# Kernel tuning notes

Measured on AMD Instinct MI355X. Metric: run time of the kernel, lower is better.

The kernel has to match this reference:

```python
import jax, jax.numpy as jnp
import numpy as np

H = 256      # HIDDEN_DIM
F_IN = 16    # input_dim
B = 512
S = 168      # encoder sequence length
T = 24       # PRED_LEN


def _lstm_cell(x, h, c, w_ih, w_hh, b):
    # torch gate order: i, f, g, o
    g = x @ w_ih.T + h @ w_hh.T + b
    i, f, gg, o = jnp.split(g, 4, axis=-1)
    c_new = jax.nn.sigmoid(f) * c + jax.nn.sigmoid(i) * jnp.tanh(gg)
    h_new = jax.nn.sigmoid(o) * jnp.tanh(c_new)
    return h_new, c_new


def _lstm_layer(x, w_ih, w_hh, b):
    # x: [S, B, in] -> outputs [S, B, H], final (h, c)
    Bv, Hv = x.shape[1], w_hh.shape[1]
    init = (jnp.zeros((Bv, Hv), x.dtype), jnp.zeros((Bv, Hv), x.dtype))
    def step(carry, xt):
        h, c = _lstm_cell(xt, carry[0], carry[1], w_ih, w_hh, b)
        return (h, c), h
    (h, c), ys = jax.lax.scan(step, init, x)
    return ys, h, c


def setup_inputs() -> dict:
    key = jax.random.key(0)
    ks = jax.random.split(key, 24)
    s = 1.0 / np.sqrt(H)
    u = lambda k, shape: jax.random.uniform(k, shape, jnp.float32, -s, s)
    inp = {}
    inp['src'] = jax.random.normal(ks[0], (B, S, F_IN), jnp.float32)
    # encoder LSTM (2 layers); biases b_ih + b_hh fused into one vector
    inp['enc_w_ih0'] = u(ks[1], (4 * H, F_IN))
    inp['enc_w_hh0'] = u(ks[2], (4 * H, H))
    inp['enc_b0'] = u(ks[3], (4 * H,))
    inp['enc_w_ih1'] = u(ks[4], (4 * H, H))
    inp['enc_w_hh1'] = u(ks[5], (4 * H, H))
    inp['enc_b1'] = u(ks[6], (4 * H,))
    # decoder LSTM (2 layers), input_size = 1 + H
    inp['dec_w_ih0'] = u(ks[7], (4 * H, 1 + H))
    inp['dec_w_hh0'] = u(ks[8], (4 * H, H))
    inp['dec_b0'] = u(ks[9], (4 * H,))
    inp['dec_w_ih1'] = u(ks[10], (4 * H, H))
    inp['dec_w_hh1'] = u(ks[11], (4 * H, H))
    inp['dec_b1'] = u(ks[12], (4 * H,))
    # attention: Linear(2H -> H), v: Linear(H -> 1, no bias), position bias
    inp['attn_w'] = u(ks[13], (H, 2 * H))
    inp['attn_b'] = u(ks[14], (H,))
    inp['attn_v'] = u(ks[15], (H,))
    inp['pos_bias'] = jax.random.normal(ks[16], (H,), jnp.float32)
    # fc_out: Linear(H -> 1)
    inp['fc_w'] = u(ks[17], (1, H))
    inp['fc_b'] = u(ks[18], (1,))
    return inp


def reference(src, enc_w_ih0, enc_w_hh0, enc_b0, enc_w_ih1, enc_w_hh1, enc_b1,
              dec_w_ih0, dec_w_hh0, dec_b0, dec_w_ih1, dec_w_hh1, dec_b1,
              attn_w, attn_b, attn_v, pos_bias, fc_w, fc_b):
    x = jnp.transpose(src, (1, 0, 2))  # [S, B, F]
    y0, _, _ = _lstm_layer(x, enc_w_ih0, enc_w_hh0, enc_b0)
    enc_out_t, h1e, c1e = _lstm_layer(y0, enc_w_ih1, enc_w_hh1, enc_b1)
    # also need final state of layer 0 for decoder init
    h0e, c0e = y0[-1], None
    # recompute layer-0 final cell state: rerun scan carry output
    # (cheap alternative: _lstm_layer returns (ys, h, c); reuse it)
    _, h0e, c0e = _lstm_layer(x, enc_w_ih0, enc_w_hh0, enc_b0)
    enc_out = jnp.transpose(enc_out_t, (1, 0, 2))  # [B, S, H]

    We, Wd = attn_w[:, :H], attn_w[:, H:]
    enc_proj = jnp.einsum('bsh,gh->bsg', enc_out, We)  # precomputed encoder projection
    dec_in0 = src[:, -1, -1:]  # [B, 1]

    def dec_step(carry, t):
        h0, c0, h1, c1, dec_in = carry
        # additive attention using top-layer decoder hidden
        e = jnp.tanh(enc_proj + (h1 @ Wd.T + attn_b)[:, None, :])
        e = e + pos_bias[None, None, :] * (t / 24.0)
        w = jax.nn.softmax(e @ attn_v, axis=1)              # [B, S]
        ctx = jnp.einsum('bs,bsh->bh', w, enc_out)          # [B, H]
        x0 = jnp.concatenate([dec_in, ctx], axis=1)          # [B, 1+H]
        h0n, c0n = _lstm_cell(x0, h0, c0, dec_w_ih0, dec_w_hh0, dec_b0)
        h1n, c1n = _lstm_cell(h0n, h1, c1, dec_w_ih1, dec_w_hh1, dec_b1)
        pred = h1n @ fc_w.T + fc_b                           # [B, 1]
        # NOTE: the gated blend of decoder_output in the source is dead code
        # (the blended tensor is never used), so it is omitted here.
        return (h0n, c0n, h1n, c1n, pred), pred

    ts = jnp.arange(T, dtype=src.dtype)
    _, preds = jax.lax.scan(dec_step, (h0e, c0e, h1e, c1e, dec_in0), ts)
    return jnp.transpose(preds, (1, 0, 2))  # [B, T, 1]
```

## Files before the change

kernel.cpp:

```cpp
#include <hip/hip_runtime.h>
#include <hip/hip_fp16.h>
#include <math.h>

#define BB 512
#define HH 256
#define SS 168
#define TT 24
#define NBLK 256
#define NTHR 512
typedef unsigned long long ull;
typedef unsigned short u16;
#define BH 131072ull

#define O_Y0  0ull
#define O_H1  262144ull
#define O_H0  524288ull
#define O_CTX 786432ull
#define O_W0  933888ull
#define O_W1  1261568ull
#define O_WP  2834432ull
#define O_WDT 2835456ull
#define O_BP  2900992ull
#define O_E16 2905088ull
#define O_P16 13915136ull

typedef float f32x4 __attribute__((ext_vector_type(4)));
typedef float v2f __attribute__((ext_vector_type(2)));
typedef unsigned int ru4 __attribute__((ext_vector_type(4)));

__device__ __forceinline__ float sigf(float x) { return 1.f / (1.f + expf(-x)); }

#define AR __ATOMIC_RELAXED
#define SCA __HIP_MEMORY_SCOPE_AGENT
__device__ __forceinline__ int aLd(int* p) { return __hip_atomic_load(p, AR, SCA); }
__device__ __forceinline__ int aAdd(int* p, int v) { return __hip_atomic_fetch_add(p, v, AR, SCA); }

__device__ __forceinline__ float2 ld2(const float* p) {
  ull raw = __hip_atomic_load((const ull*)p, AR, SCA);
  float2 v; v.x = __uint_as_float((unsigned)raw); v.y = __uint_as_float((unsigned)(raw >> 32));
  return v;
}
__device__ __forceinline__ float ld1(const float* p) {
  unsigned raw = __hip_atomic_load((const unsigned*)p, AR, SCA);
  return __uint_as_float(raw);
}
__device__ __forceinline__ void st1(float* p, float v) {
  __hip_atomic_store((unsigned*)p, __float_as_uint(v), AR, SCA);
}
__device__ __forceinline__ void sth(__half* p, __half v) {
  __hip_atomic_store((unsigned short*)p, __half_as_ushort(v), AR, SCA);
}
__device__ __forceinline__ void stu(unsigned* p, unsigned v) {
  __hip_atomic_store(p, v, AR, SCA);
}

__device__ __forceinline__ void ld_h2(const float* p, v2f& a) {
  asm volatile("global_load_dwordx2 %0, %1, off sc0 sc1"
               : "=&v"(a) : "v"(p) : "memory");
}
__device__ __forceinline__ void ld_w2(const u16* ph, const u16* pl, ru4& h, ru4& l) {
  asm volatile("global_load_dwordx4 %0, %2, off\n\t"
               "global_load_dwordx4 %1, %3, off"
               : "=&v"(h), "=&v"(l) : "v"(ph), "v"(pl) : "memory");
}
#define VMW(n) asm volatile("s_waitcnt vmcnt(" #n ")" ::: "memory")

#define MFMA(d, a, b) asm volatile("v_mfma_f32_16x16x32_bf16 %0, %1, %2, %0" \
                                   : "+v"(d) : "v"(a), "v"(b))
#define TOUCH(x) asm volatile("" : "+v"(x))

__device__ __forceinline__ void poll(int* f, int tgt) {
  while (aLd(f) < tgt) __builtin_amdgcn_s_sleep(1);
}
__device__ __forceinline__ void flag_arrive(int* f) {
  asm volatile("s_waitcnt vmcnt(0)" ::: "memory");
  __syncthreads();
  if (threadIdx.x == 0) aAdd(f, 1);
}
__device__ __forceinline__ void flag_wait2(int* f0, int t0, int* f1, int t1) {
  if (threadIdx.x == 0 && f0) poll(f0, t0);
  if (threadIdx.x == 64 && f1) poll(f1, t1);
  __syncthreads();
}

struct SMT {
  union {
    struct { unsigned WsH[128][20]; unsigned WsL[128][20]; float Ht[32][36]; } m;
    struct { float As[32][65];  float Bs[32][65]; } g;
    struct { float h1s[256], qs[256], vs[256], sc[192], ctxs[1024], sred[4]; } at;
  };
};

__device__ __forceinline__ void fma16(float acc[4][4], const float4 hv, const float4 wv) {
  acc[0][0] += hv.x * wv.x; acc[0][1] += hv.x * wv.y; acc[0][2] += hv.x * wv.z; acc[0][3] += hv.x * wv.w;
  acc[1][0] += hv.y * wv.x; acc[1][1] += hv.y * wv.y; acc[1][2] += hv.y * wv.z; acc[1][3] += hv.y * wv.w;
  acc[2][0] += hv.z * wv.x; acc[2][1] += hv.z * wv.y; acc[2][2] += hv.z * wv.z; acc[2][3] += hv.z * wv.w;
  acc[3][0] += hv.w * wv.x; acc[3][1] += hv.w * wv.y; acc[3][2] += hv.w * wv.z; acc[3][3] += hv.w * wv.w;
}

__device__ __forceinline__ unsigned rne16(unsigned u) {
  return (u + 0x7fffu + ((u >> 16) & 1u)) >> 16;
}
__device__ __forceinline__ void split8v(const f32x4 a, const f32x4 b, ru4& hi, ru4& lo) {
#pragma unroll
  for (int j = 0; j < 4; j++) {
    const float x = (j < 2) ? a[2 * j] : b[2 * j - 4];
    const float y = (j < 2) ? a[2 * j + 1] : b[2 * j - 3];
    const unsigned hx = rne16(__float_as_uint(x)), hy = rne16(__float_as_uint(y));
    const float rx = x - __uint_as_float(hx << 16);
    const float ry = y - __uint_as_float(hy << 16);
    hi[j] = (hx & 0xffffu) | (hy << 16);
    lo[j] = (rne16(__float_as_uint(rx)) & 0xffffu) | (rne16(__float_as_uint(ry)) << 16);
  }
}

__device__ __forceinline__ void comp_mfma(SMT& sm, int wq, int w1, int l15, int l4,
                                          f32x4 acc[2])
{
  const int hr = w1 * 16 + l15;
  const f32x4 hv0 = *(const f32x4*)&sm.m.Ht[hr][l4 * 8];
  const f32x4 hv1 = *(const f32x4*)&sm.m.Ht[hr][l4 * 8 + 4];
  ru4 bhi, blo;
  split8v(hv0, hv1, bhi, blo);
  asm volatile("s_nop 1" : "+v"(bhi), "+v"(blo));
#pragma unroll
  for (int g = 0; g < 2; g++) {
    const int cr = wq * 32 + g * 16 + l15;
    ru4 ah = *(const ru4*)&sm.m.WsH[cr][l4 * 4];
    ru4 al = *(const ru4*)&sm.m.WsL[cr][l4 * 4];
    MFMA(acc[g], ah, bhi);
    MFMA(acc[g], ah, blo);
    MFMA(acc[g], al, bhi);
  }
}

#define STW(wh, wl) do { \
  *(ru4*)&sm.m.WsH[cgt][kt * 4] = (wh); \
  *(ru4*)&sm.m.WsL[cgt][kt * 4] = (wl); } while (0)
#define STH(a) do { \
  sm.m.Ht[r][p2 * 2] = (a)[0]; sm.m.Ht[r][p2 * 2 + 1] = (a)[1]; } while (0)

__device__ void gemm_pipe(const u16* wbh, const u16* wbl,
                          const float* hb0, const float* hb1,
                          int NC, int nc0, f32x4 acc[2], SMT& sm,
                          int wq, int w1, int l15, int l4)
{
  const int tid = threadIdx.x;
  const int r = tid & 31, p2 = tid >> 5;
  const int cgt = tid & 127, kt = tid >> 7;
  const float* h1p = hb1 - (ull)nc0 * 32;
#define HBk(k) (((k) < nc0) ? (hb0 + (k) * 32) : (h1p + (k) * 32))
  ru4 wh0, wl0, wh1, wl1, wh2, wl2, wh3, wl3;
  v2f h0, h1, h2, h3;
  ld_w2(wbh,      wbl,      wh0, wl0);
  ld_h2(HBk(0), h0);
  ld_w2(wbh + 32, wbl + 32, wh1, wl1);
  ld_h2(HBk(1), h1);
  ld_h2(HBk(2), h2);
  for (int c = 0; c < NC; c += 4) {
    VMW(4);
    STW(wh0, wl0); STH(h0);
    __syncthreads();
    ld_w2(wbh + (c + 2) * 32, wbl + (c + 2) * 32, wh2, wl2);
    ld_h2(HBk(c + 3), h3);
    comp_mfma(sm, wq, w1, l15, l4, acc);
    __syncthreads();
    VMW(4);
    STW(wh1, wl1); STH(h1);
    __syncthreads();
    ld_w2(wbh + (c + 3) * 32, wbl + (c + 3) * 32, wh3, wl3);
    ld_h2(HBk(c + 4), h0);
    comp_mfma(sm, wq, w1, l15, l4, acc);
    __syncthreads();
    VMW(4);
    STW(wh2, wl2); STH(h2);
    __syncthreads();
    ld_w2(wbh + (c + 4) * 32, wbl + (c + 4) * 32, wh0, wl0);
    ld_h2(HBk(c + 5), h1);
    comp_mfma(sm, wq, w1, l15, l4, acc);
    __syncthreads();
    VMW(4);
    STW(wh3, wl3); STH(h3);
    __syncthreads();
    ld_w2(wbh + (c + 5) * 32, wbl + (c + 5) * 32, wh1, wl1);
    ld_h2(HBk(c + 6), h2);
    comp_mfma(sm, wq, w1, l15, l4, acc);
    __syncthreads();
  }
  asm volatile("s_waitcnt vmcnt(0)" ::: "memory");
  asm volatile("s_nop 7\n\ts_nop 7" : "+v"(acc[0]), "+v"(acc[1]));
#undef HBk
}

__device__ __forceinline__ void lstm_epi2(f32x4 acc[2], float cR[2], int row, int ubase, int l4,
                                          float* hout, __half* e16, int sstep)
{
#pragma unroll
  for (int g = 0; g < 2; g++) {
    const int u = ubase + g * 4 + l4;
    const float iv = sigf(acc[g][0]), fv = sigf(acc[g][1]);
    const float gv = tanhf(acc[g][2]), ov = sigf(acc[g][3]);
    const float cn = fv * cR[g] + iv * gv;
    cR[g] = cn;
    const float hn = ov * tanhf(cn);
    st1(hout + (ull)row * 256 + u, hn);
    if (e16) sth(e16 + ((ull)row * SS + sstep) * 256 + u, __float2half(hn));
  }
}

__device__ void attn_fc(int row, int t, int slot, const float* h1r, const float* wdT,
                        const float* attn_b, const float* attn_v,
                        const __half* P16, const __half* E16,
                        const float* fc_w, const float* fc_b,
                        float* ctxb, float* out, SMT& sm)
{
  const int tid = threadIdx.x;
  __syncthreads();
  if (tid < 128) {
    float2 v = ld2(h1r + (ull)slot * BH + (ull)row * 256 + tid * 2);
    sm.at.h1s[tid * 2] = v.x; sm.at.h1s[tid * 2 + 1] = v.y;
  }
  __syncthreads();
  if (t >= 1 && tid < 64) {
    float a = 0.f;
#pragma unroll
    for (int j = 0; j < 4; j++) a += sm.at.h1s[tid + 64 * j] * fc_w[tid + 64 * j];
#pragma unroll
    for (int m = 32; m >= 1; m >>= 1) a += __shfl_xor(a, m, 64);
    if (tid == 0) {
      const float p = a + fc_b[0];
      out[(ull)row * TT + (t - 1)] = p;
      st1(ctxb + (ull)row * 288 + 256, p);
    }
  }
  if (t >= TT) return;
  if (tid < 256) {
    float qv = attn_b[tid];
    for (int k = 0; k < 256; k += 4) {
      qv += sm.at.h1s[k]     * wdT[(ull)(k)     * 256 + tid];
      qv += sm.at.h1s[k + 1] * wdT[(ull)(k + 1) * 256 + tid];
      qv += sm.at.h1s[k + 2] * wdT[(ull)(k + 2) * 256 + tid];
      qv += sm.at.h1s[k + 3] * wdT[(ull)(k + 3) * 256 + tid];
    }
    sm.at.qs[tid] = qv;
    sm.at.vs[tid] = attn_v[tid];
  }
  __syncthreads();
  const int wv = tid >> 6, lane = tid & 63;
  for (int s = wv; s < SS; s += 8) {
    const __half2* Pr = (const __half2*)(P16 + ((ull)row * SS + s) * 256);
    float a = 0.f;
#pragma unroll
    for (int jj = 0; jj < 2; jj++) {
      const int i2 = lane + 64 * jj;
      const float2 pv = __half22float2(Pr[i2]);
      const int g0 = i2 * 2;
      a += sm.at.vs[g0] * tanhf(pv.x + sm.at.qs[g0]);
      a += sm.at.vs[g0 + 1] * tanhf(pv.y + sm.at.qs[g0 + 1]);
    }
#pragma unroll
    for (int m = 32; m >= 1; m >>= 1) a += __shfl_xor(a, m, 64);
    if (lane == 0) sm.at.sc[s] = a;
  }
  __syncthreads();
  if (tid < 64) {
    float m = -1e30f;
    for (int i = tid; i < SS; i += 64) m = fmaxf(m, sm.at.sc[i]);
#pragma unroll
    for (int mm = 32; mm >= 1; mm >>= 1) m = fmaxf(m, __shfl_xor(m, mm, 64));
    if (tid == 0) sm.at.sred[0] = m;
  }
  __syncthreads();
  const float smax = sm.at.sred[0];
  if (tid < SS) sm.at.sc[tid] = expf(sm.at.sc[tid] - smax);
  __syncthreads();
  if (tid < 64) {
    float ssum = 0.f;
    for (int i = tid; i < SS; i += 64) ssum += sm.at.sc[i];
#pragma unroll
    for (int mm = 32; mm >= 1; mm >>= 1) ssum += __shfl_xor(ssum, mm, 64);
    if (tid == 0) sm.at.sred[1] = ssum;
  }
  __syncthreads();
  const float rinv = 1.f / sm.at.sred[1];
  const int u2 = tid & 127, sh = tid >> 7;
  float cx = 0.f, cy = 0.f;
  for (int s = sh * 42; s < sh * 42 + 42; s++) {
    const float w = sm.at.sc[s] * rinv;
    const float2 ev = __half22float2(*(const __half2*)(E16 + ((ull)row * SS + s) * 256 + u2 * 2));
    cx += w * ev.x; cy += w * ev.y;
  }
  sm.at.ctxs[sh * 256 + u2 * 2] = cx;
  sm.at.ctxs[sh * 256 + u2 * 2 + 1] = cy;
  __syncthreads();
  if (tid < 256)
    st1(ctxb + (ull)row * 288 + tid,
        sm.at.ctxs[tid] + sm.at.ctxs[256 + tid] + sm.at.ctxs[512 + tid] + sm.at.ctxs[768 + tid]);
}

__device__ void proj_tile(const __half* E16, const float* attn_w, __half* P16,
                          int m0, int n0, SMT& sm)
{
  const int tid = threadIdx.x;
  const bool act = tid < 256;
  const int mq = tid & 15, nq = (tid >> 4) & 15;
  const int li = tid & 63, kq = (tid >> 6) & 3;
  float acc[4][4] = {{0.f}};
  for (int k0 = 0; k0 < 256; k0 += 32) {
    if (act) {
      float4 raw = *(const float4*)(E16 + (ull)(m0 + li) * 256 + k0 + kq * 8);
      const __half* hp = (const __half*)&raw;
#pragma unroll
      for (int i = 0; i < 8; i++) sm.g.As[kq * 8 + i][li] = __half2float(hp[i]);
      const float* gb = attn_w + (ull)(n0 + li) * 512 + k0 + kq * 8;
      const float4 v0 = *(const float4*)gb, v1 = *(const float4*)(gb + 4);
      sm.g.Bs[kq * 8 + 0][li] = v0.x; sm.g.Bs[kq * 8 + 1][li] = v0.y;
      sm.g.Bs[kq * 8 + 2][li] = v0.z; sm.g.Bs[kq * 8 + 3][li] = v0.w;
      sm.g.Bs[kq * 8 + 4][li] = v1.x; sm.g.Bs[kq * 8 + 5][li] = v1.y;
      sm.g.Bs[kq * 8 + 6][li] = v1.z; sm.g.Bs[kq * 8 + 7][li] = v1.w;
    }
    __syncthreads();
    if (act) {
#pragma unroll 8
      for (int kk = 0; kk < 32; kk++) {
        const float4 a4 = *(const float4*)&sm.g.As[kk][mq * 4];
        const float4 b4 = *(const float4*)&sm.g.Bs[kk][nq * 4];
        fma16(acc, a4, b4);
      }
    }
    __syncthreads();
  }
  if (act) {
#pragma unroll
    for (int i = 0; i < 4; i++) {
      const int m = m0 + mq * 4 + i;
#pragma unroll
      for (int j = 0; j < 2; j++) {
        __half2 h2; h2.x = __float2half(acc[i][j * 2]); h2.y = __float2half(acc[i][j * 2 + 1]);
        stu((unsigned*)(P16 + (ull)m * 256 + n0 + nq * 4) + j, *(unsigned*)&h2);
      }
    }
  }
}

__global__ __launch_bounds__(512, 1) void seq2seq_pipe(
    const float* __restrict__ src,
    const float* __restrict__ attn_w, const float* __restrict__ attn_b,
    const float* __restrict__ attn_v,
    const float* __restrict__ fc_w, const float* __restrict__ fc_b,
    float* __restrict__ out, int* __restrict__ ib)
{
  __shared__ SMT sm;
  const int blk = blockIdx.x;
  const int tid = threadIdx.x;
  float* fb = (float*)ib + 65536;
  float* y0r  = fb + O_Y0;
  float* h1r  = fb + O_H1;
  float* h0r  = fb + O_H0;
  float* zb   = h0r + BH;
  float* ctxb = fb + O_CTX;
  const u16* whi0 = (const u16*)(fb + O_W0);
  const u16* wlo0 = whi0 + 1024ull * 320;
  const u16* whi1 = (const u16*)(fb + O_W1);
  const u16* wlo1 = whi1 + 1024ull * 512;
  const u16* dhi0 = whi1 + 2ull * 1024 * 512;
  const u16* dlo0 = whi1 + 3ull * 1024 * 512;
  const u16* dhi1 = whi1 + 4ull * 1024 * 512;
  const u16* dlo1 = whi1 + 5ull * 1024 * 512;
  const float* wp  = fb + O_WP;
  const float* wdT = fb + O_WDT;
  const float* bp  = fb + O_BP;
  __half* E16 = (__half*)(fb + O_E16);
  __half* P16 = (__half*)(fb + O_P16);
  const int g = blk >> 5, m = blk & 31;
  const int rowg = g * 64;
  int* gf = ib + g * 1024;
  int* ife = gf;
  int* ifa = gf + 704; int* ifh0 = gf + 736; int* ifh1 = gf + 768; int* ifp = gf + 900;

  const int lm = (m < 16) ? m : (m - 16);
  const int row0 = rowg + (lm & 1) * 32;
  const int gc0 = (lm >> 1) * 128;
  const int w = tid >> 6;
  const int l15 = tid & 15, l4 = (tid >> 4) & 3;
  const int w1 = w & 1, wq = w >> 1;
  const int gcw = gc0 + wq * 32;
  const int myrow = row0 + w1 * 16 + l15;
  const int ubase = gcw >> 2;
  const int r = tid & 31;
  const int cgt = tid & 127, kt = tid >> 7;

  float cReg[2] = {0.f, 0.f};

  for (int t = 0; t <= SS; t++) {
    flag_wait2(t ? ife + (t - 1) : nullptr, 32, nullptr, 0);
    if (m < 16) {
      if (t < SS) {
        f32x4 acc[2];
#pragma unroll
        for (int gg = 0; gg < 2; gg++) {
          acc[gg] = *(const f32x4*)(bp + gcw + gg * 16 + l4 * 4);
          TOUCH(acc[gg]);
        }
        {
          ru4 wxh, wxl;
          ld_w2(whi0 + (ull)(gc0 + cgt) * 320 + kt * 8,
                wlo0 + (ull)(gc0 + cgt) * 320 + kt * 8, wxh, wxl);
          VMW(0);
          *(ru4*)&sm.m.WsH[cgt][kt * 4] = wxh;
          *(ru4*)&sm.m.WsL[cgt][kt * 4] = wxl;
          const int f = tid >> 5;
          sm.m.Ht[r][f]      = src[((ull)(row0 + r) * SS + t) * 16 + f];
          sm.m.Ht[r][f + 16] = 0.f;
          __syncthreads();
          comp_mfma(sm, wq, w1, l15, l4, acc);
          __syncthreads();
        }
        const float* ysrc = (t == 0) ? zb : (y0r + (ull)((t + 1) & 1) * BH);
        const float* hb0 = ysrc + (ull)(row0 + r) * 256 + (tid >> 5) * 2;
        gemm_pipe(whi0 + (ull)(gc0 + cgt) * 320 + 32 + kt * 8,
                  wlo0 + (ull)(gc0 + cgt) * 320 + 32 + kt * 8,
                  hb0, hb0, 8, 8, acc, sm, wq, w1, l15, l4);
        lstm_epi2(acc, cReg, myrow, ubase, l4, y0r + (ull)(t & 1) * BH, nullptr, 0);
      }
    } else {
      if (t >= 1) {
        const int s = t - 1;
        f32x4 acc[2];
#pragma unroll
        for (int gg = 0; gg < 2; gg++) {
          acc[gg] = *(const f32x4*)(bp + 1024 + gcw + gg * 16 + l4 * 4);
          TOUCH(acc[gg]);
        }
        const float* ysrc = y0r + (ull)(s & 1) * BH;
        const float* hsrc = (s == 0) ? zb : (h1r + (ull)((s + 1) & 1) * BH);
        const float* hb0 = ysrc + (ull)(row0 + r) * 256 + (tid >> 5) * 2;
        const float* hb1 = hsrc + (ull)(row0 + r) * 256 + (tid >> 5) * 2;
        gemm_pipe(whi1 + (ull)(gc0 + cgt) * 512 + kt * 8,
                  wlo1 + (ull)(gc0 + cgt) * 512 + kt * 8,
                  hb0, hb1, 16, 8, acc, sm, wq, w1, l15, l4);
        lstm_epi2(acc, cReg, myrow, ubase, l4, h1r + (ull)(s & 1) * BH, E16, s);
      }
    }
    flag_arrive(ife + t);
  }

  if (tid == 0) poll(ife + SS, 32);
  __syncthreads();
  {
    const int em0 = rowg * SS;
    for (int tau = m; tau < 672; tau += 32)
      proj_tile(E16, attn_w, P16, em0 + (tau >> 2) * 64, (tau & 3) * 64, sm);
  }
  flag_arrive(ifp);

  for (int t = 0; t <= TT; t++) {
    if (t == 0) flag_wait2(ifp, 32, nullptr, 0);
    else flag_wait2(ifh1 + (t - 1), 16, nullptr, 0);
    const int slot = (t + 1) & 1;
    attn_fc(rowg + 2 * m,     t, slot, h1r, wdT, attn_b, attn_v, P16, E16, fc_w, fc_b, ctxb, out, sm);
    attn_fc(rowg + 2 * m + 1, t, slot, h1r, wdT, attn_b, attn_v, P16, E16, fc_w, fc_b, ctxb, out, sm);
    if (t == TT) break;
    flag_arrive(ifa + t);
    if (m < 16) {
      flag_wait2(ifa + t, 32, t ? ifh0 + (t - 1) : nullptr, 16);
      f32x4 acc[2];
#pragma unroll
      for (int gg = 0; gg < 2; gg++) {
        acc[gg] = *(const f32x4*)(bp + 2048 + gcw + gg * 16 + l4 * 4);
        TOUCH(acc[gg]);
      }
      const float* h0src = (t == 0) ? (y0r + BH) : (h0r + (ull)((t + 1) & 1) * BH);
      const float* hb0 = ctxb + (ull)(row0 + r) * 288 + (tid >> 5) * 2;
      const float* hb1 = h0src + (ull)(row0 + r) * 256 + (tid >> 5) * 2;
      gemm_pipe(dhi0 + (ull)(gc0 + cgt) * 512 + kt * 8,
                dlo0 + (ull)(gc0 + cgt) * 512 + kt * 8,
                hb0, hb1, 16, 8, acc, sm, wq, w1, l15, l4);
      const float p = ld1(ctxb + (ull)myrow * 288 + 256);
#pragma unroll
      for (int gg = 0; gg < 2; gg++) {
        const f32x4 wpv = *(const f32x4*)(wp + gcw + gg * 16 + l4 * 4);
        acc[gg] = acc[gg] + wpv * p;
      }
      lstm_epi2(acc, cReg, myrow, ubase, l4, h0r + (ull)(t & 1) * BH, nullptr, 0);
      flag_arrive(ifh0 + t);
    } else {
      flag_wait2(ifh0 + t, 16, t ? ifh1 + (t - 1) : nullptr, 16);
      f32x4 acc[2];
#pragma unroll
      for (int gg = 0; gg < 2; gg++) {
        acc[gg] = *(const f32x4*)(bp + 3072 + gcw + gg * 16 + l4 * 4);
        TOUCH(acc[gg]);
      }
      const float* hb0 = h0r + (ull)(t & 1) * BH + (ull)(row0 + r) * 256 + (tid >> 5) * 2;
      const float* hb1 = h1r + (ull)((t + 1) & 1) * BH + (ull)(row0 + r) * 256 + (tid >> 5) * 2;
      gemm_pipe(dhi1 + (ull)(gc0 + cgt) * 512 + kt * 8,
                dlo1 + (ull)(gc0 + cgt) * 512 + kt * 8,
                hb0, hb1, 16, 8, acc, sm, wq, w1, l15, l4);
      lstm_epi2(acc, cReg, myrow, ubase, l4, h1r + (ull)(t & 1) * BH, nullptr, 0);
      flag_arrive(ifh1 + t);
    }
  }
}

__device__ __forceinline__ void split_store(float v, u16* hi, u16* lo, ull i) {
  const unsigned u = __float_as_uint(v);
  const unsigned hb = (u + 0x7fffu + ((u >> 16) & 1u)) >> 16;
  const float rr = v - __uint_as_float(hb << 16);
  const unsigned ur = __float_as_uint(rr);
  const unsigned lb = (ur + 0x7fffu + ((ur >> 16) & 1u)) >> 16;
  hi[i] = (u16)hb; lo[i] = (u16)lb;
}

__global__ void init_all(
    const float* __restrict__ src,
    const float* __restrict__ ewih0, const float* __restrict__ ewhh0, const float* __restrict__ eb0,
    const float* __restrict__ ewih1, const float* __restrict__ ewhh1, const float* __restrict__ eb1,
    const float* __restrict__ dwih0, const float* __restrict__ dwhh0, const float* __restrict__ db0,
    const float* __restrict__ dwih1, const float* __restrict__ dwhh1, const float* __restrict__ db1,
    const float* __restrict__ attn_w, int* __restrict__ ib)
{
  const int gid = blockIdx.x * 256 + threadIdx.x;
  const int NG = 1024 * 256;
  float* fb = (float*)ib + 65536;
  u16* whi0 = (u16*)(fb + O_W0);
  u16* wlo0 = whi0 + 1024ull * 320;
  u16* whi1 = (u16*)(fb + O_W1);
  u16* wlo1 = whi1 + 1024ull * 512;
  u16* dhi0 = whi1 + 2ull * 1024 * 512;
  u16* dlo0 = whi1 + 3ull * 1024 * 512;
  u16* dhi1 = whi1 + 4ull * 1024 * 512;
  u16* dlo1 = whi1 + 5ull * 1024 * 512;
  float* wpd = fb + O_WP;

  for (int i = gid; i < 8192; i += NG) ib[i] = 0;
  for (int i = gid; i < (int)BH; i += NG) fb[O_H0 + BH + i] = 0.f;
  for (int i = gid; i < 1024 * 320; i += NG) {
    const int cg = i / 320, k = i - cg * 320, j = (cg & 3) * 256 + (cg >> 2);
    float v = 0.f;
    if (k < 16) v = ewih0[(ull)j * 16 + k];
    else if (k >= 32 && k < 288) v = ewhh0[(ull)j * 256 + (k - 32)];
    split_store(v, whi0, wlo0, i);
  }
  for (int i = gid; i < 1024 * 512; i += NG) {
    const int cg = i >> 9, k = i & 511, j = (cg & 3) * 256 + (cg >> 2);
    split_store((k < 256) ? ewih1[(ull)j * 256 + k] : ewhh1[(ull)j * 256 + k - 256], whi1, wlo1, i);
    split_store((k < 256) ? dwih0[(ull)j * 257 + 1 + k] : dwhh0[(ull)j * 256 + k - 256], dhi0, dlo0, i);
    split_store((k < 256) ? dwih1[(ull)j * 256 + k] : dwhh1[(ull)j * 256 + k - 256], dhi1, dlo1, i);
  }
  for (int i = gid; i < 1024; i += NG) {
    const int j = (i & 3) * 256 + (i >> 2);
    wpd[i] = dwih0[(ull)j * 257];
  }
  for (int i = gid; i < 256 * 256; i += NG) {
    const int k = i >> 8, gg = i & 255;
    fb[O_WDT + i] = attn_w[(ull)gg * 512 + 256 + k];
  }
  for (int i = gid; i < 4096; i += NG) {
    const int set = i >> 10, cg = i & 1023, j = (cg & 3) * 256 + (cg >> 2);
    const float* bsrc = (set == 0) ? eb0 : (set == 1) ? eb1 : (set == 2) ? db0 : db1;
    fb[O_BP + i] = bsrc[j];
  }
  for (int i = gid; i < 512; i += NG)
    fb[O_CTX + (ull)i * 288 + 256] = src[((ull)i * SS + 167) * 16 + 15];
}

extern "C" void kernel_launch(void* const* d_in, const int* in_sizes, int n_in,
                              void* d_out, int out_size, void* d_ws, size_t ws_size,
                              hipStream_t stream)
{
  const float* src    = (const float*)d_in[0];
  const float* ewih0  = (const float*)d_in[1];
  const float* ewhh0  = (const float*)d_in[2];
  const float* eb0    = (const float*)d_in[3];
  const float* ewih1  = (const float*)d_in[4];
  const float* ewhh1  = (const float*)d_in[5];
  const float* eb1    = (const float*)d_in[6];
  const float* dwih0  = (const float*)d_in[7];
  const float* dwhh0  = (const float*)d_in[8];
  const float* db0    = (const float*)d_in[9];
  const float* dwih1  = (const float*)d_in[10];
  const float* dwhh1  = (const float*)d_in[11];
  const float* db1    = (const float*)d_in[12];
  const float* attn_w = (const float*)d_in[13];
  const float* attn_b = (const float*)d_in[14];
  const float* attn_v = (const float*)d_in[15];
  const float* fc_w   = (const float*)d_in[17];
  const float* fc_b   = (const float*)d_in[18];
  float* out = (float*)d_out;
  int* ib    = (int*)d_ws;

  init_all<<<1024, 256, 0, stream>>>(src, ewih0, ewhh0, eb0, ewih1, ewhh1, eb1,
                                     dwih0, dwhh0, db0, dwih1, dwhh1, db1, attn_w, ib);

  void* args[] = {
    (void*)&src, (void*)&attn_w, (void*)&attn_b, (void*)&attn_v,
    (void*)&fc_w, (void*)&fc_b, (void*)&out, (void*)&ib,
  };
  hipError_t lerr = hipLaunchCooperativeKernel((const void*)seq2seq_pipe, dim3(NBLK), dim3(NTHR),
                                               args, 0, stream);
  if (lerr != hipSuccess) {
    hipLaunchKernelGGL(seq2seq_pipe, dim3(NBLK), dim3(NTHR), 0, stream,
                       src, attn_w, attn_b, attn_v, fc_w, fc_b, out, ib);
  }
}
```

Measured before the change: 7.029 ms.

## Replace atomic counter barriers with per-block padded flag slots polled by a wavefront

Replaces the shared fetch-add counters used as inter-block barriers with one monotonic flag slot per producer block, each padded to its own stride. Each waiter polls all relevant slots in parallel across the 64 lanes of one wavefront and proceeds when every slot reaches the target. In the encoder, blocks now wait only on the 16 producer blocks covering their own row half rather than all 32 in the group. The aim is to remove atomic contention on a single counter and cut unnecessary dependencies. The cost is more flag memory, a larger zero-initialised flag region, and more polling loads per wait.

```diff
diff --git a/kernel.cpp b/kernel.cpp
--- a/kernel.cpp
+++ b/kernel.cpp
@@ -32,8 +32,7 @@
 
 #define AR __ATOMIC_RELAXED
 #define SCA __HIP_MEMORY_SCOPE_AGENT
-__device__ __forceinline__ int aLd(int* p) { return __hip_atomic_load(p, AR, SCA); }
-__device__ __forceinline__ int aAdd(int* p, int v) { return __hip_atomic_fetch_add(p, v, AR, SCA); }
+__device__ __forceinline__ int aLd(const int* p) { return __hip_atomic_load(p, AR, SCA); }
 
 __device__ __forceinline__ float2 ld2(const float* p) {
   ull raw = __hip_atomic_load((const ull*)p, AR, SCA);
@@ -69,17 +68,35 @@
                                    : "+v"(d) : "v"(a), "v"(b))
 #define TOUCH(x) asm volatile("" : "+v"(x))
 
-__device__ __forceinline__ void poll(int* f, int tgt) {
-  while (aLd(f) < tgt) __builtin_amdgcn_s_sleep(1);
-}
-__device__ __forceinline__ void flag_arrive(int* f) {
+#define SSTR 16
+__device__ __forceinline__ void arrive_slot(int* slot, int val) {
   asm volatile("s_waitcnt vmcnt(0)" ::: "memory");
   __syncthreads();
-  if (threadIdx.x == 0) aAdd(f, 1);
-}
-__device__ __forceinline__ void flag_wait2(int* f0, int t0, int* f1, int t1) {
-  if (threadIdx.x == 0 && f0) poll(f0, t0);
-  if (threadIdx.x == 64 && f1) poll(f1, t1);
+  if (threadIdx.x == 0) __hip_atomic_store(slot, val, AR, SCA);
+}
+__device__ __forceinline__ void wait_slots(const int* base, int n, int tgt) {
+  if (threadIdx.x < 64) {
+    const int lane = threadIdx.x;
+    const int* p = base + lane * SSTR;
+    for (;;) {
+      const int ok = (lane >= n) || (aLd(p) >= tgt);
+      if (__all(ok)) break;
+      __builtin_amdgcn_s_sleep(1);
+    }
+  }
+  __syncthreads();
+}
+__device__ __forceinline__ void wait_slots2(const int* a, int na, const int* b, int nb, int tgt) {
+  if (threadIdx.x < 64) {
+    const int lane = threadIdx.x;
+    const int* p = (lane < na) ? (a + lane * SSTR)
+                 : (lane < na + nb) ? (b + (lane - na) * SSTR) : (const int*)nullptr;
+    for (;;) {
+      const int ok = (p == nullptr) || (aLd(p) >= tgt);
+      if (__all(ok)) break;
+      __builtin_amdgcn_s_sleep(1);
+    }
+  }
   __syncthreads();
 }
 
@@ -374,13 +391,18 @@
   __half* P16 = (__half*)(fb + O_P16);
   const int g = blk >> 5, m = blk & 31;
   const int rowg = g * 64;
-  int* gf = ib + g * 1024;
-  int* ife = gf;
-  int* ifa = gf + 704; int* ifh0 = gf + 736; int* ifh1 = gf + 768; int* ifp = gf + 900;
+  int* gf = ib + g * 4096;
+  int* f_e0 = gf;
+  int* f_e1 = gf + 256;
+  int* f_pr = gf + 512;
+  int* f_a  = gf + 1024;
+  int* f_h0 = gf + 1536;
+  int* f_h1 = gf + 1792;
 
   const int lm = (m < 16) ? m : (m - 16);
-  const int row0 = rowg + (lm & 1) * 32;
-  const int gc0 = (lm >> 1) * 128;
+  const int rh = lm & 1, gi = lm >> 1;
+  const int row0 = rowg + rh * 32;
+  const int gc0 = gi * 128;
   const int w = tid >> 6;
   const int l15 = tid & 15, l4 = (tid >> 4) & 3;
   const int w1 = w & 1, wq = w >> 1;
@@ -390,10 +412,14 @@
   const int r = tid & 31;
   const int cgt = tid & 127, kt = tid >> 7;
 
+  int* my_enc_slot = (m < 16 ? f_e0 : f_e1) + (rh * 8 + gi) * SSTR;
+  const int* e0h = f_e0 + rh * 8 * SSTR;
+  const int* e1h = f_e1 + rh * 8 * SSTR;
+
   float cReg[2] = {0.f, 0.f};
 
   for (int t = 0; t <= SS; t++) {
-    flag_wait2(t ? ife + (t - 1) : nullptr, 32, nullptr, 0);
+    if (t) wait_slots2(e0h, 8, e1h, 8, t);
     if (m < 16) {
       if (t < SS) {
         f32x4 acc[2];
@@ -442,28 +468,28 @@
         lstm_epi2(acc, cReg, myrow, ubase, l4, h1r + (ull)(s & 1) * BH, E16, s);
       }
     }
-    flag_arrive(ife + t);
-  }
-
-  if (tid == 0) poll(ife + SS, 32);
-  __syncthreads();
+    arrive_slot(my_enc_slot, t + 1);
+  }
+
+  wait_slots(f_e1, 16, SS + 1);
   {
     const int em0 = rowg * SS;
     for (int tau = m; tau < 672; tau += 32)
       proj_tile(E16, attn_w, P16, em0 + (tau >> 2) * 64, (tau & 3) * 64, sm);
   }
-  flag_arrive(ifp);
+  arrive_slot(f_pr + m * SSTR, 1);
 
   for (int t = 0; t <= TT; t++) {
-    if (t == 0) flag_wait2(ifp, 32, nullptr, 0);
-    else flag_wait2(ifh1 + (t - 1), 16, nullptr, 0);
+    if (t == 0) wait_slots(f_pr, 32, 1);
+    else wait_slots(f_h1, 16, t);
     const int slot = (t + 1) & 1;
     attn_fc(rowg + 2 * m,     t, slot, h1r, wdT, attn_b, attn_v, P16, E16, fc_w, fc_b, ctxb, out, sm);
     attn_fc(rowg + 2 * m + 1, t, slot, h1r, wdT, attn_b, attn_v, P16, E16, fc_w, fc_b, ctxb, out, sm);
     if (t == TT) break;
-    flag_arrive(ifa + t);
+    arrive_slot(f_a + m * SSTR, t + 1);
     if (m < 16) {
-      flag_wait2(ifa + t, 32, t ? ifh0 + (t - 1) : nullptr, 16);
+      wait_slots(f_a, 32, t + 1);
+      if (t) wait_slots(f_h0, 16, t);
       f32x4 acc[2];
 #pragma unroll
       for (int gg = 0; gg < 2; gg++) {
@@ -483,9 +509,10 @@
         acc[gg] = acc[gg] + wpv * p;
       }
       lstm_epi2(acc, cReg, myrow, ubase, l4, h0r + (ull)(t & 1) * BH, nullptr, 0);
-      flag_arrive(ifh0 + t);
+      arrive_slot(f_h0 + m * SSTR, t + 1);
     } else {
-      flag_wait2(ifh0 + t, 16, t ? ifh1 + (t - 1) : nullptr, 16);
+      wait_slots(f_h0, 16, t + 1);
+      if (t) wait_slots(f_h1, 16, t);
       f32x4 acc[2];
 #pragma unroll
       for (int gg = 0; gg < 2; gg++) {
@@ -498,7 +525,7 @@
                 dlo1 + (ull)(gc0 + cgt) * 512 + kt * 8,
                 hb0, hb1, 16, 8, acc, sm, wq, w1, l15, l4);
       lstm_epi2(acc, cReg, myrow, ubase, l4, h1r + (ull)(t & 1) * BH, nullptr, 0);
-      flag_arrive(ifh1 + t);
+      arrive_slot(f_h1 + (m - 16) * SSTR, t + 1);
     }
   }
 }
@@ -533,7 +560,7 @@
   u16* dlo1 = whi1 + 5ull * 1024 * 512;
   float* wpd = fb + O_WP;
 
-  for (int i = gid; i < 8192; i += NG) ib[i] = 0;
+  for (int i = gid; i < 32768; i += NG) ib[i] = 0;
   for (int i = gid; i < (int)BH; i += NG) fb[O_H0 + BH + i] = 0.f;
   for (int i = gid; i < 1024 * 320; i += NG) {
     const int cg = i / 320, k = i - cg * 320, j = (cg & 3) * 256 + (cg >> 2);
```

Result: faster. 6.599 ms (-6.1%).
